# Optimization experiments

Hardware: AMD Instinct MI355X
Metric: run time of the kernel (lower is better)

Reference implementation:

```python
import jax, jax.numpy as jnp
import numpy as np

N_NODES = 100000
N_EDGES = 500000
IN_DIM = 16
HEADS = 4
OUT_DIM = 128  # per head; concat=True -> 512 total
NEG_SLOPE = 0.2


def setup_inputs() -> dict:
    key = jax.random.key(0)
    ks = jax.random.split(key, 6)
    node_edge_feat = jax.random.normal(ks[0], (N_NODES, IN_DIM), dtype=jnp.float32)
    node_to_node_index = jax.random.randint(ks[1], (2, N_EDGES), 0, N_NODES, dtype=jnp.int32)
    s = 1.0 / np.sqrt(IN_DIM)
    W_l = jax.random.normal(ks[2], (IN_DIM, HEADS * OUT_DIM), dtype=jnp.float32) * s
    W_r = jax.random.normal(ks[3], (IN_DIM, HEADS * OUT_DIM), dtype=jnp.float32) * s
    b_l = jnp.zeros((HEADS * OUT_DIM,), jnp.float32)
    b_r = jnp.zeros((HEADS * OUT_DIM,), jnp.float32)
    att = jax.random.normal(ks[4], (HEADS, OUT_DIM), dtype=jnp.float32) * (1.0 / np.sqrt(OUT_DIM))
    bias = jnp.zeros((HEADS * OUT_DIM,), jnp.float32)
    return {
        "node_edge_feat": node_edge_feat,
        "node_to_node_index": node_to_node_index,
        "W_l": W_l, "b_l": b_l, "W_r": W_r, "b_r": b_r,
        "att": att, "bias": bias,
    }


def reference(node_edge_feat, node_to_node_index, W_l, b_l, W_r, b_r, att, bias):
    """GATv2Conv forward (eval mode, dropout off), concat=True."""
    N = node_edge_feat.shape[0]
    src = node_to_node_index[0]  # message source j
    dst = node_to_node_index[1]  # aggregation target i
    x_l = (node_edge_feat @ W_l + b_l).reshape(N, HEADS, OUT_DIM)
    x_r = (node_edge_feat @ W_r + b_r).reshape(N, HEADS, OUT_DIM)
    # per-edge GATv2 score: a^T LeakyReLU(x_l[j] + x_r[i])
    m = jax.nn.leaky_relu(x_l[src] + x_r[dst], NEG_SLOPE)  # [E, H, C]
    e = jnp.einsum('ehc,hc->eh', m, att)                   # [E, H]
    # segment softmax over incoming edges of each target node
    emax = jax.lax.stop_gradient(jax.ops.segment_max(e, dst, num_segments=N))[dst]
    ex = jnp.exp(e - emax)
    denom = jax.ops.segment_sum(ex, dst, num_segments=N)[dst]
    alpha = ex / denom                                     # [E, H]
    # scatter-aggregate alpha-weighted source features
    out = jax.ops.segment_sum(alpha[:, :, None] * x_l[src], dst, num_segments=N)
    return out.reshape(N, HEADS * OUT_DIM) + bias
```

## Files before the change

kernel.cpp:

```cpp
#include <hip/hip_runtime.h>
#include <hip/hip_fp16.h>
#include <math.h>

#define HEADS 4
#define OUT_DIM 128
#define HC 512
#define IN_DIM 16
#define NEG_SLOPE 0.2f
#define NPB 64
#define FNPB 64

__global__ __launch_bounds__(256) void proj_kernel(
    const float* __restrict__ x,
    const float* __restrict__ Wl, const float* __restrict__ bl,
    const float* __restrict__ Wr, const float* __restrict__ br,
    __half* __restrict__ xl, __half* __restrict__ xr, int N)
{
    __shared__ float xs[NPB * IN_DIM];
    const int t = threadIdx.x;
    const int c0 = t * 2;

    float wl0[IN_DIM], wl1[IN_DIM], wr0[IN_DIM], wr1[IN_DIM];
#pragma unroll
    for (int k = 0; k < IN_DIM; ++k) {
        float2 a = *(const float2*)&Wl[k * HC + c0];
        wl0[k] = a.x; wl1[k] = a.y;
        float2 b = *(const float2*)&Wr[k * HC + c0];
        wr0[k] = b.x; wr1[k] = b.y;
    }
    const float2 blv = *(const float2*)&bl[c0];
    const float2 brv = *(const float2*)&br[c0];

    const int base = blockIdx.x * NPB;
    if (base >= N) return;
    const int nn = min(NPB, N - base);
    for (int i = t; i < nn * IN_DIM; i += 256) xs[i] = x[base * IN_DIM + i];
    __syncthreads();

    for (int u = 0; u < nn; ++u) {
        const float* xv = &xs[u * IN_DIM];
        float a0 = blv.x, a1 = blv.y, r0 = brv.x, r1 = brv.y;
#pragma unroll
        for (int k = 0; k < IN_DIM; ++k) {
            const float xk = xv[k];
            a0 = fmaf(xk, wl0[k], a0);
            a1 = fmaf(xk, wl1[k], a1);
            r0 = fmaf(xk, wr0[k], r0);
            r1 = fmaf(xk, wr1[k], r1);
        }
        const size_t n = base + u;
        *(__half2*)&xl[n * HC + c0] = __floats2half2_rn(a0, a1);
        *(__half2*)&xr[n * HC + c0] = __floats2half2_rn(r0, r1);
    }
}

__global__ __launch_bounds__(256) void hist_kernel(
    const int* __restrict__ idx, int* __restrict__ counts, int E)
{
    const int e = blockIdx.x * 256 + threadIdx.x;
    if (e < E) atomicAdd(&counts[idx[E + e]], 1);
}

__global__ __launch_bounds__(1024) void scan1_kernel(
    const int* __restrict__ counts, int* __restrict__ starts,
    int* __restrict__ blocksums, int N)
{
    __shared__ int wsum[16];
    const int t = threadIdx.x;
    const int g = blockIdx.x * 1024 + t;
    const int v = (g < N) ? counts[g] : 0;
    int xi = v;
#pragma unroll
    for (int o = 1; o < 64; o <<= 1) {
        const int y = __shfl_up(xi, o);
        if ((t & 63) >= o) xi += y;
    }
    if ((t & 63) == 63) wsum[t >> 6] = xi;
    __syncthreads();
    if (t < 16) {
        const int w = wsum[t];
        int xx = w;
#pragma unroll
        for (int o = 1; o < 16; o <<= 1) {
            const int y = __shfl_up(xx, o);
            if (t >= o) xx += y;
        }
        wsum[t] = xx - w;
        if (t == 15) blocksums[blockIdx.x] = xx;
    }
    __syncthreads();
    if (g < N) starts[g] = xi - v + wsum[t >> 6];
}

__global__ __launch_bounds__(128) void scan2_kernel(int* __restrict__ blocksums, int nb)
{
    __shared__ int sm[128];
    const int t = threadIdx.x;
    const int v = (t < nb) ? blocksums[t] : 0;
    sm[t] = v;
    __syncthreads();
    for (int o = 1; o < 128; o <<= 1) {
        const int a = (t >= o) ? sm[t - o] : 0;
        __syncthreads();
        sm[t] += a;
        __syncthreads();
    }
    if (t < nb) blocksums[t] = sm[t] - v;
}

__global__ __launch_bounds__(256) void scan3_kernel(
    int* __restrict__ starts, const int* __restrict__ blocksums,
    int* __restrict__ cursor, int N)
{
    const int i = blockIdx.x * 256 + threadIdx.x;
    if (i < N) {
        const int s = starts[i] + blocksums[i >> 10];
        starts[i] = s;
        cursor[i] = s;
    }
}

__global__ __launch_bounds__(256) void fill_kernel(
    const int* __restrict__ idx, int* __restrict__ cursor,
    int* __restrict__ esrc, int E)
{
    const int e = blockIdx.x * 256 + threadIdx.x;
    if (e < E) {
        const int dst = idx[E + e];
        const int p = atomicAdd(&cursor[dst], 1);
        esrc[p] = idx[e];
    }
}

__device__ __forceinline__ void h8_to_f(const uint4 u, float4& a, float4& b)
{
    const __half2* hp = (const __half2*)&u;
    const float2 f0 = __half22float2(hp[0]);
    const float2 f1 = __half22float2(hp[1]);
    const float2 f2 = __half22float2(hp[2]);
    const float2 f3 = __half22float2(hp[3]);
    a = make_float4(f0.x, f0.y, f1.x, f1.y);
    b = make_float4(f2.x, f2.y, f3.x, f3.y);
}

__global__ __launch_bounds__(256) void agg_kernel(
    const int* __restrict__ esrc, const int* __restrict__ starts,
    const int* __restrict__ counts,
    const __half* __restrict__ xl, const __half* __restrict__ xr,
    const float* __restrict__ xraw, const float* __restrict__ att,
    float* __restrict__ ynorm, float* __restrict__ denout, int N)
{
    const int gid = blockIdx.x * 256 + threadIdx.x;
    const int n = gid >> 6;
    if (n >= N) return;
    const int lane = threadIdx.x & 63;
    const int k = lane & 15;

    const uint4 ur = *(const uint4*)(xr + (size_t)n * HC + lane * 8);
    float4 b0, b1;
    h8_to_f(ur, b0, b1);
    const float4* atp = (const float4*)att;
    const float4 t0 = atp[lane * 2 + 0];
    const float4 t1 = atp[lane * 2 + 1];

    const int k0  = __builtin_amdgcn_readfirstlane(starts[n]);
    const int deg = __builtin_amdgcn_readfirstlane(counts[n]);

    float y = 0.f, den = 0.f;
    uint4 rA = make_uint4(0, 0, 0, 0), rB = make_uint4(0, 0, 0, 0);
    float xkA = 0.f, xkB = 0.f;
    if (deg > 0) {
        const int s = __builtin_amdgcn_readfirstlane(esrc[k0]);
        rA  = *(const uint4*)(xl + (size_t)s * HC + lane * 8);
        xkA = xraw[s * IN_DIM + k];
    }
    if (deg > 1) {
        const int s = __builtin_amdgcn_readfirstlane(esrc[k0 + 1]);
        rB  = *(const uint4*)(xl + (size_t)s * HC + lane * 8);
        xkB = xraw[s * IN_DIM + k];
    }
    for (int i = 0; i < deg; ++i) {
        const uint4 rc = rA; const float xk = xkA;
        rA = rB; xkA = xkB;
        if (i + 2 < deg) {
            const int s = __builtin_amdgcn_readfirstlane(esrc[k0 + i + 2]);
            rB  = *(const uint4*)(xl + (size_t)s * HC + lane * 8);
            xkB = xraw[s * IN_DIM + k];
        }
        float4 a0, a1;
        h8_to_f(rc, a0, a1);
        float sc = 0.f, z;
        z = a0.x + b0.x; sc = fmaf(t0.x, (z > 0.f ? z : NEG_SLOPE * z), sc);
        z = a0.y + b0.y; sc = fmaf(t0.y, (z > 0.f ? z : NEG_SLOPE * z), sc);
        z = a0.z + b0.z; sc = fmaf(t0.z, (z > 0.f ? z : NEG_SLOPE * z), sc);
        z = a0.w + b0.w; sc = fmaf(t0.w, (z > 0.f ? z : NEG_SLOPE * z), sc);
        z = a1.x + b1.x; sc = fmaf(t1.x, (z > 0.f ? z : NEG_SLOPE * z), sc);
        z = a1.y + b1.y; sc = fmaf(t1.y, (z > 0.f ? z : NEG_SLOPE * z), sc);
        z = a1.z + b1.z; sc = fmaf(t1.z, (z > 0.f ? z : NEG_SLOPE * z), sc);
        z = a1.w + b1.w; sc = fmaf(t1.w, (z > 0.f ? z : NEG_SLOPE * z), sc);
#pragma unroll
        for (int o = 1; o < 16; o <<= 1) sc += __shfl_xor(sc, o);
        const float ex = __expf(sc);
        den += ex;
        y = fmaf(ex, xk, y);
    }

    const float inv = den > 0.f ? 1.f / den : 0.f;
    ynorm[(size_t)n * 64 + lane] = y * inv;
    if (k == 0) denout[(size_t)n * 4 + (lane >> 4)] = den;
}

__global__ __launch_bounds__(256) void final_kernel(
    const float* __restrict__ ynorm, const float* __restrict__ den,
    const float* __restrict__ Wl, const float* __restrict__ bl,
    const float* __restrict__ bias, float* __restrict__ out, int N)
{
    __shared__ float ys[FNPB * 64];
    __shared__ float dsm[FNPB * 4];
    const int t = threadIdx.x;
    const int c0 = t * 2;
    const int h = t >> 6;

    float w0[IN_DIM], w1[IN_DIM];
#pragma unroll
    for (int k = 0; k < IN_DIM; ++k) {
        const float2 a = *(const float2*)&Wl[k * HC + c0];
        w0[k] = a.x; w1[k] = a.y;
    }
    const float blc0 = bl[c0],   blc1 = bl[c0 + 1];
    const float bsc0 = bias[c0], bsc1 = bias[c0 + 1];

    const int base = blockIdx.x * FNPB;
    if (base >= N) return;
    const int nn = min(FNPB, N - base);
    for (int i = t; i < nn * 16; i += 256)
        ((float4*)ys)[i] = ((const float4*)(ynorm + (size_t)base * 64))[i];
    for (int i = t; i < nn * 4; i += 256) dsm[i] = den[(size_t)base * 4 + i];
    __syncthreads();

    for (int u = 0; u < nn; ++u) {
        const float* yr = &ys[u * 64 + h * 16];
        const float g = dsm[u * 4 + h] > 0.f ? 1.f : 0.f;
        float o0 = fmaf(g, blc0, bsc0);
        float o1 = fmaf(g, blc1, bsc1);
#pragma unroll
        for (int kk = 0; kk < IN_DIM; ++kk) {
            const float yv = yr[kk];
            o0 = fmaf(yv, w0[kk], o0);
            o1 = fmaf(yv, w1[kk], o1);
        }
        *(float2*)&out[(size_t)(base + u) * HC + c0] = make_float2(o0, o1);
    }
}

extern "C" void kernel_launch(void* const* d_in, const int* in_sizes, int n_in,
                              void* d_out, int out_size, void* d_ws, size_t ws_size,
                              hipStream_t stream)
{
    const float* x    = (const float*)d_in[0];
    const int*   idx  = (const int*)d_in[1];
    const float* Wl   = (const float*)d_in[2];
    const float* bl   = (const float*)d_in[3];
    const float* Wr   = (const float*)d_in[4];
    const float* br   = (const float*)d_in[5];
    const float* att  = (const float*)d_in[6];
    const float* bias = (const float*)d_in[7];

    const int N = in_sizes[0] / IN_DIM;
    const int E = in_sizes[1] / 2;

    __half* xl16     = (__half*)d_ws;
    __half* xr16     = xl16 + (size_t)N * HC;
    float*  ynorm    = (float*)(xr16 + (size_t)N * HC);
    float*  den      = ynorm + (size_t)N * 64;
    int*    counts   = (int*)(den + (size_t)N * 4);
    int*    starts   = counts + N;
    int*    cursor   = starts + N;
    int*    blocksums= cursor + N;
    int*    esrc     = blocksums + 128;
    float*  outf     = (float*)d_out;

    const int nb = (N + 1023) / 1024;

    hipMemsetAsync(counts, 0, (size_t)N * sizeof(int), stream);

    proj_kernel<<<(N + NPB - 1) / NPB, 256, 0, stream>>>(x, Wl, bl, Wr, br, xl16, xr16, N);

    hist_kernel<<<(E + 255) / 256, 256, 0, stream>>>(idx, counts, E);
    scan1_kernel<<<nb, 1024, 0, stream>>>(counts, starts, blocksums, N);
    scan2_kernel<<<1, 128, 0, stream>>>(blocksums, nb);
    scan3_kernel<<<(N + 255) / 256, 256, 0, stream>>>(starts, blocksums, cursor, N);
    fill_kernel<<<(E + 255) / 256, 256, 0, stream>>>(idx, cursor, esrc, E);

    agg_kernel<<<(N * 64 + 255) / 256, 256, 0, stream>>>(
        esrc, starts, counts, xl16, xr16, x, att, ynorm, den, N);

    final_kernel<<<(N + FNPB - 1) / FNPB, 256, 0, stream>>>(
        ynorm, den, Wl, bl, bias, outf, N);
}
```

Before: 440.6 us.

## Replace CSR build with fixed-capacity per-node buckets plus spill path

Removes the histogram, three-pass scan and cursor fill in favor of a single atomic fill into per-destination buckets of capacity 64, with overflow edges sent to a spill list. The spill list is handled by a separate atomic-accumulation kernel. Normalization by the softmax denominator moves into the final kernel so that spill contributions can be added to unnormalized sums. The aggregation prefetch depth also grows from two to three edges. The cost is a larger workspace, a sparse bucket layout, and an extra kernel launch.

```diff
diff --git a/kernel.cpp b/kernel.cpp
--- a/kernel.cpp
+++ b/kernel.cpp
@@ -9,6 +9,7 @@
 #define NEG_SLOPE 0.2f
 #define NPB 64
 #define FNPB 64
+#define KCAP 64
 
 __global__ __launch_bounds__(256) void proj_kernel(
     const float* __restrict__ x,
@@ -54,81 +55,23 @@
     }
 }
 
-__global__ __launch_bounds__(256) void hist_kernel(
-    const int* __restrict__ idx, int* __restrict__ counts, int E)
-{
-    const int e = blockIdx.x * 256 + threadIdx.x;
-    if (e < E) atomicAdd(&counts[idx[E + e]], 1);
-}
-
-__global__ __launch_bounds__(1024) void scan1_kernel(
-    const int* __restrict__ counts, int* __restrict__ starts,
-    int* __restrict__ blocksums, int N)
-{
-    __shared__ int wsum[16];
-    const int t = threadIdx.x;
-    const int g = blockIdx.x * 1024 + t;
-    const int v = (g < N) ? counts[g] : 0;
-    int xi = v;
-#pragma unroll
-    for (int o = 1; o < 64; o <<= 1) {
-        const int y = __shfl_up(xi, o);
-        if ((t & 63) >= o) xi += y;
-    }
-    if ((t & 63) == 63) wsum[t >> 6] = xi;
-    __syncthreads();
-    if (t < 16) {
-        const int w = wsum[t];
-        int xx = w;
-#pragma unroll
-        for (int o = 1; o < 16; o <<= 1) {
-            const int y = __shfl_up(xx, o);
-            if (t >= o) xx += y;
-        }
-        wsum[t] = xx - w;
-        if (t == 15) blocksums[blockIdx.x] = xx;
-    }
-    __syncthreads();
-    if (g < N) starts[g] = xi - v + wsum[t >> 6];
-}
-
-__global__ __launch_bounds__(128) void scan2_kernel(int* __restrict__ blocksums, int nb)
-{
-    __shared__ int sm[128];
-    const int t = threadIdx.x;
-    const int v = (t < nb) ? blocksums[t] : 0;
-    sm[t] = v;
-    __syncthreads();
-    for (int o = 1; o < 128; o <<= 1) {
-        const int a = (t >= o) ? sm[t - o] : 0;
-        __syncthreads();
-        sm[t] += a;
-        __syncthreads();
-    }
-    if (t < nb) blocksums[t] = sm[t] - v;
-}
-
-__global__ __launch_bounds__(256) void scan3_kernel(
-    int* __restrict__ starts, const int* __restrict__ blocksums,
-    int* __restrict__ cursor, int N)
-{
-    const int i = blockIdx.x * 256 + threadIdx.x;
-    if (i < N) {
-        const int s = starts[i] + blocksums[i >> 10];
-        starts[i] = s;
-        cursor[i] = s;
-    }
-}
-
-__global__ __launch_bounds__(256) void fill_kernel(
-    const int* __restrict__ idx, int* __restrict__ cursor,
-    int* __restrict__ esrc, int E)
+__global__ __launch_bounds__(256) void fillb_kernel(
+    const int* __restrict__ idx, int* __restrict__ counts,
+    int* __restrict__ esrcb, int* __restrict__ spill, int* __restrict__ spillcnt,
+    int E)
 {
     const int e = blockIdx.x * 256 + threadIdx.x;
     if (e < E) {
-        const int dst = idx[E + e];
-        const int p = atomicAdd(&cursor[dst], 1);
-        esrc[p] = idx[e];
+        const int dst  = idx[E + e];
+        const int src  = idx[e];
+        const int slot = atomicAdd(&counts[dst], 1);
+        if (slot < KCAP) {
+            esrcb[dst * KCAP + slot] = src;
+        } else {
+            const int sp = atomicAdd(spillcnt, 1);
+            spill[2 * sp]     = dst;
+            spill[2 * sp + 1] = src;
+        }
     }
 }
 
@@ -144,11 +87,10 @@
 }
 
 __global__ __launch_bounds__(256) void agg_kernel(
-    const int* __restrict__ esrc, const int* __restrict__ starts,
-    const int* __restrict__ counts,
+    const int* __restrict__ esrcb, const int* __restrict__ counts,
     const __half* __restrict__ xl, const __half* __restrict__ xr,
     const float* __restrict__ xraw, const float* __restrict__ att,
-    float* __restrict__ ynorm, float* __restrict__ denout, int N)
+    float* __restrict__ yraw, float* __restrict__ denout, int N)
 {
     const int gid = blockIdx.x * 256 + threadIdx.x;
     const int n = gid >> 6;
@@ -163,29 +105,30 @@
     const float4 t0 = atp[lane * 2 + 0];
     const float4 t1 = atp[lane * 2 + 1];
 
-    const int k0  = __builtin_amdgcn_readfirstlane(starts[n]);
-    const int deg = __builtin_amdgcn_readfirstlane(counts[n]);
+    const int deg  = min(KCAP, __builtin_amdgcn_readfirstlane(counts[n]));
+    const int base = n * KCAP;
 
     float y = 0.f, den = 0.f;
-    uint4 rA = make_uint4(0, 0, 0, 0), rB = make_uint4(0, 0, 0, 0);
-    float xkA = 0.f, xkB = 0.f;
+    uint4 rA = {0,0,0,0}, rB = {0,0,0,0}, rC = {0,0,0,0};
+    float qA = 0.f, qB = 0.f, qC = 0.f;
     if (deg > 0) {
-        const int s = __builtin_amdgcn_readfirstlane(esrc[k0]);
-        rA  = *(const uint4*)(xl + (size_t)s * HC + lane * 8);
-        xkA = xraw[s * IN_DIM + k];
+        const int s = __builtin_amdgcn_readfirstlane(esrcb[base]);
+        rA = *(const uint4*)(xl + (size_t)s * HC + lane * 8); qA = xraw[s * IN_DIM + k];
     }
     if (deg > 1) {
-        const int s = __builtin_amdgcn_readfirstlane(esrc[k0 + 1]);
-        rB  = *(const uint4*)(xl + (size_t)s * HC + lane * 8);
-        xkB = xraw[s * IN_DIM + k];
+        const int s = __builtin_amdgcn_readfirstlane(esrcb[base + 1]);
+        rB = *(const uint4*)(xl + (size_t)s * HC + lane * 8); qB = xraw[s * IN_DIM + k];
+    }
+    if (deg > 2) {
+        const int s = __builtin_amdgcn_readfirstlane(esrcb[base + 2]);
+        rC = *(const uint4*)(xl + (size_t)s * HC + lane * 8); qC = xraw[s * IN_DIM + k];
     }
     for (int i = 0; i < deg; ++i) {
-        const uint4 rc = rA; const float xk = xkA;
-        rA = rB; xkA = xkB;
-        if (i + 2 < deg) {
-            const int s = __builtin_amdgcn_readfirstlane(esrc[k0 + i + 2]);
-            rB  = *(const uint4*)(xl + (size_t)s * HC + lane * 8);
-            xkB = xraw[s * IN_DIM + k];
+        const uint4 rc = rA; const float xk = qA;
+        rA = rB; qA = qB; rB = rC; qB = qC;
+        if (i + 3 < deg) {
+            const int s = __builtin_amdgcn_readfirstlane(esrcb[base + i + 3]);
+            rC = *(const uint4*)(xl + (size_t)s * HC + lane * 8); qC = xraw[s * IN_DIM + k];
         }
         float4 a0, a1;
         h8_to_f(rc, a0, a1);
@@ -205,13 +148,50 @@
         y = fmaf(ex, xk, y);
     }
 
-    const float inv = den > 0.f ? 1.f / den : 0.f;
-    ynorm[(size_t)n * 64 + lane] = y * inv;
+    yraw[(size_t)n * 64 + lane] = y;
     if (k == 0) denout[(size_t)n * 4 + (lane >> 4)] = den;
 }
 
+__global__ __launch_bounds__(256) void spill_kernel(
+    const int* __restrict__ spill, const int* __restrict__ spillcnt,
+    const __half* __restrict__ xl, const __half* __restrict__ xr,
+    const float* __restrict__ xraw, const float* __restrict__ att,
+    float* __restrict__ yraw, float* __restrict__ den)
+{
+    const int nsp  = spillcnt[0];
+    const int wid  = (blockIdx.x * 256 + threadIdx.x) >> 6;
+    const int nw   = (gridDim.x * 256) >> 6;
+    const int lane = threadIdx.x & 63;
+    const int k = lane & 15;
+    if (wid >= nsp && nsp == 0) return;
+    const float4* atp = (const float4*)att;
+    const float4 t0 = atp[lane * 2 + 0];
+    const float4 t1 = atp[lane * 2 + 1];
+    for (int sp = wid; sp < nsp; sp += nw) {
+        const int dst = __builtin_amdgcn_readfirstlane(spill[2 * sp]);
+        const int src = __builtin_amdgcn_readfirstlane(spill[2 * sp + 1]);
+        float4 a0, a1, b0, b1;
+        h8_to_f(*(const uint4*)(xl + (size_t)src * HC + lane * 8), a0, a1);
+        h8_to_f(*(const uint4*)(xr + (size_t)dst * HC + lane * 8), b0, b1);
+        float sc = 0.f, z;
+        z = a0.x + b0.x; sc = fmaf(t0.x, (z > 0.f ? z : NEG_SLOPE * z), sc);
+        z = a0.y + b0.y; sc = fmaf(t0.y, (z > 0.f ? z : NEG_SLOPE * z), sc);
+        z = a0.z + b0.z; sc = fmaf(t0.z, (z > 0.f ? z : NEG_SLOPE * z), sc);
+        z = a0.w + b0.w; sc = fmaf(t0.w, (z > 0.f ? z : NEG_SLOPE * z), sc);
+        z = a1.x + b1.x; sc = fmaf(t1.x, (z > 0.f ? z : NEG_SLOPE * z), sc);
+        z = a1.y + b1.y; sc = fmaf(t1.y, (z > 0.f ? z : NEG_SLOPE * z), sc);
+        z = a1.z + b1.z; sc = fmaf(t1.z, (z > 0.f ? z : NEG_SLOPE * z), sc);
+        z = a1.w + b1.w; sc = fmaf(t1.w, (z > 0.f ? z : NEG_SLOPE * z), sc);
+#pragma unroll
+        for (int o = 1; o < 16; o <<= 1) sc += __shfl_xor(sc, o);
+        const float ex = __expf(sc);
+        atomicAdd(&yraw[(size_t)dst * 64 + lane], ex * xraw[src * IN_DIM + k]);
+        if (k == 0) atomicAdd(&den[(size_t)dst * 4 + (lane >> 4)], ex);
+    }
+}
+
 __global__ __launch_bounds__(256) void final_kernel(
-    const float* __restrict__ ynorm, const float* __restrict__ den,
+    const float* __restrict__ yraw, const float* __restrict__ den,
     const float* __restrict__ Wl, const float* __restrict__ bl,
     const float* __restrict__ bias, float* __restrict__ out, int N)
 {
@@ -234,22 +214,25 @@
     if (base >= N) return;
     const int nn = min(FNPB, N - base);
     for (int i = t; i < nn * 16; i += 256)
-        ((float4*)ys)[i] = ((const float4*)(ynorm + (size_t)base * 64))[i];
+        ((float4*)ys)[i] = ((const float4*)(yraw + (size_t)base * 64))[i];
     for (int i = t; i < nn * 4; i += 256) dsm[i] = den[(size_t)base * 4 + i];
     __syncthreads();
 
     for (int u = 0; u < nn; ++u) {
         const float* yr = &ys[u * 64 + h * 16];
-        const float g = dsm[u * 4 + h] > 0.f ? 1.f : 0.f;
-        float o0 = fmaf(g, blc0, bsc0);
-        float o1 = fmaf(g, blc1, bsc1);
+        const float d = dsm[u * 4 + h];
+        const float inv = d > 0.f ? 1.f / d : 0.f;
+        const float g   = d > 0.f ? 1.f : 0.f;
+        float o0 = 0.f, o1 = 0.f;
 #pragma unroll
         for (int kk = 0; kk < IN_DIM; ++kk) {
             const float yv = yr[kk];
             o0 = fmaf(yv, w0[kk], o0);
             o1 = fmaf(yv, w1[kk], o1);
         }
-        *(float2*)&out[(size_t)(base + u) * HC + c0] = make_float2(o0, o1);
+        const float r0 = fmaf(o0, inv, fmaf(g, blc0, bsc0));
+        const float r1 = fmaf(o1, inv, fmaf(g, blc1, bsc1));
+        *(float2*)&out[(size_t)(base + u) * HC + c0] = make_float2(r0, r1);
     }
 }
 
@@ -271,30 +254,25 @@
 
     __half* xl16     = (__half*)d_ws;
     __half* xr16     = xl16 + (size_t)N * HC;
-    float*  ynorm    = (float*)(xr16 + (size_t)N * HC);
-    float*  den      = ynorm + (size_t)N * 64;
+    float*  yraw     = (float*)(xr16 + (size_t)N * HC);
+    float*  den      = yraw + (size_t)N * 64;
     int*    counts   = (int*)(den + (size_t)N * 4);
-    int*    starts   = counts + N;
-    int*    cursor   = starts + N;
-    int*    blocksums= cursor + N;
-    int*    esrc     = blocksums + 128;
+    int*    spillcnt = counts + N;
+    int*    esrcb    = spillcnt + 1;
+    int*    spill    = esrcb + (size_t)N * KCAP;
     float*  outf     = (float*)d_out;
 
-    const int nb = (N + 1023) / 1024;
-
-    hipMemsetAsync(counts, 0, (size_t)N * sizeof(int), stream);
+    hipMemsetAsync(counts, 0, (size_t)(N + 1) * sizeof(int), stream);
 
     proj_kernel<<<(N + NPB - 1) / NPB, 256, 0, stream>>>(x, Wl, bl, Wr, br, xl16, xr16, N);
 
-    hist_kernel<<<(E + 255) / 256, 256, 0, stream>>>(idx, counts, E);
-    scan1_kernel<<<nb, 1024, 0, stream>>>(counts, starts, blocksums, N);
-    scan2_kernel<<<1, 128, 0, stream>>>(blocksums, nb);
-    scan3_kernel<<<(N + 255) / 256, 256, 0, stream>>>(starts, blocksums, cursor, N);
-    fill_kernel<<<(E + 255) / 256, 256, 0, stream>>>(idx, cursor, esrc, E);
+    fillb_kernel<<<(E + 255) / 256, 256, 0, stream>>>(idx, counts, esrcb, spill, spillcnt, E);
 
     agg_kernel<<<(N * 64 + 255) / 256, 256, 0, stream>>>(
-        esrc, starts, counts, xl16, xr16, x, att, ynorm, den, N);
+        esrcb, counts, xl16, xr16, x, att, yraw, den, N);
+
+    spill_kernel<<<256, 256, 0, stream>>>(spill, spillcnt, xl16, xr16, x, att, yraw, den);
 
     final_kernel<<<(N + FNPB - 1) / FNPB, 256, 0, stream>>>(
-        ynorm, den, Wl, bl, bias, outf, N);
-}
+        yraw, den, Wl, bl, bias, outf, N);
+}
```

New measurement: 435.9 us. No clear change (-1.1%).
